# Performance work log

Hardware: AMD Instinct MI355X
Metric: run time of the kernel (lower is better)

Reference implementation:

```python
import jax, jax.numpy as jnp
import numpy as np

BASIS_N = 3            # Cl(3,0): 3 generators, euclidean metric e_i^2 = +1
BASIS_DIM = 1 << BASIS_N  # 8


def _geometric_product_table(n=BASIS_N):
    """G[i, j, k] such that e_i * e_j = sum_k G[i,j,k] e_k for blades indexed by bitmask."""
    dim = 1 << n
    G = np.zeros((dim, dim, dim), dtype=np.float32)
    for a in range(dim):
        for b in range(dim):
            # canonical reordering sign (count transpositions to sort basis vectors)
            s, t = 0, a >> 1
            while t:
                s += bin(t & b).count('1')
                t >>= 1
            sign = -1.0 if (s & 1) else 1.0
            G[a, b, a ^ b] = sign  # euclidean metric: squared generators contribute +1
    return G


def setup_inputs() -> dict:
    key = jax.random.key(0)
    kx, kw, kb = jax.random.split(key, 3)
    B, Cin, Cout, D, H, Wd, K = 8, 8, 8, 48, 48, 48, 3
    x = jax.random.normal(kx, (B, Cin, BASIS_DIM, D, H, Wd), dtype=jnp.float32)
    # W: [k0, k1, k2, in_channels, out_channels, basis_dim]
    W = jax.random.normal(kw, (K, K, K, Cin, Cout, BASIS_DIM), dtype=jnp.float32) * 0.05
    b = jax.random.normal(kb, (Cout, BASIS_DIM), dtype=jnp.float32) * 0.05
    G = jnp.asarray(_geometric_product_table())
    return {"x": x, "W": W, "b": b, "G": G}


def reference(x, W, b, G):
    # out[b,o,k,d,h,w] = sum_{i,j,c,m,l,v} G[i,j,k] * x[b,c,i,d+m,h+l,w+v] * W[m,l,v,c,o,j] + b[o,k]
    # Fold the GA multiplication table into the weights, then run a single dense 3D conv
    # over the fused (channel*basis) axis -- avoids the im2col unfold intermediate.
    k0, k1, k2, cin, cout, bd = W.shape
    B, C, I, D, H, Wd = x.shape
    Wt = jnp.einsum('ijk,mlvcoj->okcimlv', G, W)          # [o, k, c, i, m, l, v]
    xr = x.reshape(B, C * I, D, H, Wd)                    # fuse channel & basis-in
    kern = Wt.reshape(cout * bd, C * I, k0, k1, k2)       # fuse out-channel & basis-out
    out = jax.lax.conv_general_dilated(
        xr, kern, window_strides=(1, 1, 1), padding='VALID',
        dimension_numbers=('NCDHW', 'OIDHW', 'NCDHW'))
    out = out.reshape(B, cout, bd, *out.shape[2:])        # [B, o, k, d, h, w]
    return out + b[None, :, :, None, None, None]
```

## Files before the change

### kernel.cpp

```cpp
#include <hip/hip_runtime.h>


namespace {

constexpr int DIN = 48, DOUT = 46;
constexpr size_t X_ELEMS = 8ull * 8 * 8 * DIN * DIN * DIN;
constexpr size_t XBF_BYTES = X_ELEMS * 2;
constexpr int APK_ELEMS = 54 * 4 * 64 * 8;
constexpr int ROW_SHORTS = 2 * 4 * 48 * 8;
constexpr int ROW_BYTES = ROW_SHORTS * 2;

__host__ __device__ constexpr int popc_(int v) { int c = 0; while (v) { c += v & 1; v >>= 1; } return c; }
__host__ __device__ inline float ga_sign(int a, int b) {
  int s = 0;
  for (int t = a >> 1; t; t >>= 1) s += popc_(t & b);
  return (s & 1) ? -1.0f : 1.0f;
}

__device__ inline unsigned short f2bf(float f) {
  unsigned u = __builtin_bit_cast(unsigned, f);
  u += 0x7fffu + ((u >> 16) & 1u);
  return (unsigned short)(u >> 16);
}

__device__ inline void gload_lds16(const void* g, void* l) {
  __builtin_amdgcn_global_load_lds(
      (const __attribute__((address_space(1))) unsigned int*)g,
      (__attribute__((address_space(3))) unsigned int*)l, 16, 0, 0);
}

using frag  = __attribute__((ext_vector_type(8))) short;
using f32x4 = __attribute__((ext_vector_type(4))) float;

__global__ __launch_bounds__(256) void cvt_x(const float* __restrict__ x,
                                             unsigned short* __restrict__ xt) {
  const int bid = blockIdx.x;
  const int yg = bid % 6, bz = bid / 6;
  const int b = bz / 48, z = bz % 48;
  const int tid = threadIdx.x;
  __shared__ __attribute__((aligned(16))) unsigned short T[8 * ROW_SHORTS];
  const float* src = x + (size_t)b * 64 * 110592 + (size_t)z * 2304 + (size_t)yg * 384;
#pragma unroll
  for (int it = 0; it < 24; ++it) {
    const int i = it * 256 + tid;
    const int k = i / 96, j = i - k * 96;
    const int y = j / 12, x4 = j - y * 12;
    float4 f = *(const float4*)(src + (size_t)k * 110592 + y * 48 + x4 * 4);
    const int cb = k >> 5, q = (k >> 3) & 3, t = k & 7;
    const int basek = ((y * 2 + cb) * 4 + q) * 384 + t;
    unsigned short bfv[4] = {f2bf(f.x), f2bf(f.y), f2bf(f.z), f2bf(f.w)};
#pragma unroll
    for (int dx = 0; dx < 4; ++dx) {
      const int xx = x4 * 4 + dx;
      T[basek + ((xx ^ y) << 3)] = bfv[dx];
    }
  }
  __syncthreads();
  uint4* dst = (uint4*)(xt + ((size_t)bz * 48 + yg * 8) * ROW_SHORTS);
#pragma unroll
  for (int it = 0; it < 12; ++it) {
    const int C = it * 256 + tid;
    const int y = C / 384;
    const unsigned byteoff = (unsigned)(C * 16) ^ (unsigned)(y << 4);
    dst[C] = *(const uint4*)((const char*)T + byteoff);
  }
}

__global__ __launch_bounds__(256) void build_apk(const float* __restrict__ W,
                                                 unsigned short* __restrict__ Apk) {
  int e = blockIdx.x * 256 + threadIdx.x;
  int t  = e & 7;
  int mi = (e >> 3) & 63;
  int q  = (e >> 9) & 3;
  int s  = e >> 11;
  int cb = s & 1, mlv = s >> 1;
  int v = mlv % 3, l = (mlv / 3) % 3, m = mlv / 9;
  int kl = cb * 32 + q * 8 + t;
  int c = kl >> 3, i = kl & 7;
  int o = mi >> 3, kb = mi & 7, j = i ^ kb;
  float val = ga_sign(i, j) * W[((((m * 3 + l) * 3 + v) * 8 + c) * 8 + o) * 8 + j];
  Apk[e] = f2bf(val);
}

__global__ __launch_bounds__(256, 2) void gpconv_mfma(
    const unsigned short* __restrict__ xt,
    const unsigned short* __restrict__ Apk,
    const float* __restrict__ bias,
    float* __restrict__ out)
{
  const int d = blockIdx.x, hg = blockIdx.y, b = blockIdx.z;
  const int h0 = hg * 8;
  const int tid = threadIdx.x;
  const int wv = tid >> 6;
  const int lane = tid & 63, r = lane & 15, q = lane >> 4;

  __shared__ __attribute__((aligned(16))) unsigned short Xs[10 * ROW_SHORTS + 32];

  f32x4 acc[4][2][3];
#pragma unroll
  for (int ms = 0; ms < 4; ++ms)
#pragma unroll
    for (int row = 0; row < 2; ++row)
#pragma unroll
      for (int nt = 0; nt < 3; ++nt) acc[ms][row][nt] = (f32x4){0.f, 0.f, 0.f, 0.f};

  const unsigned short* Apl = Apk + q * 512 + r * 8;

  auto stage_half = [&](int zin, int cb) {
    const size_t R0 = (size_t)(b * 48 + zin) * 48 + h0;
#pragma unroll
    for (int i = 0; i < 3; ++i) {
      const int row = wv + i * 4;
      if (row < 10) {
        const char* g = (const char*)xt + (R0 + row) * ROW_BYTES + cb * 3072 + (size_t)lane * 16;
        unsigned loff = (unsigned)__builtin_amdgcn_readfirstlane(row * ROW_BYTES + cb * 3072);
#pragma unroll
        for (int ip = 0; ip < 3; ++ip)
          gload_lds16(g + ip * 1024, (char*)Xs + loff + ip * 1024);
      }
    }
  };

  auto compute_half = [&](int m, int cb) {
    const unsigned short* Xb = Xs + cb * 1536 + q * 384;
#pragma unroll
    for (int l = 0; l < 3; ++l) {
#pragma unroll
      for (int v = 0; v < 3; ++v) {
        const int mlv = (m * 3 + l) * 3 + v;
        frag a[4];
#pragma unroll
        for (int ms = 0; ms < 4; ++ms)
          a[ms] = *(const frag*)(Apl + (size_t)mlv * 4096 + cb * 2048 + ms * 128);
        frag bfr[2][3];
#pragma unroll
        for (int row = 0; row < 2; ++row) {
          const unsigned short* Xrow = Xb + (wv * 2 + row + l) * ROW_SHORTS + (r + v) * 8;
#pragma unroll
          for (int nt = 0; nt < 3; ++nt)
            bfr[row][nt] = *(const frag*)(Xrow + nt * 128);
        }
#pragma unroll
        for (int ms = 0; ms < 4; ++ms)
#pragma unroll
          for (int row = 0; row < 2; ++row)
#pragma unroll
            for (int nt = 0; nt < 3; ++nt)
              acc[ms][row][nt] = __builtin_amdgcn_mfma_f32_16x16x32_bf16(
                  a[ms], bfr[row][nt], acc[ms][row][nt], 0, 0, 0);
      }
    }
  };

  stage_half(d, 0);
  stage_half(d, 1);
  __syncthreads();
#pragma unroll 1
  for (int m = 0; m < 3; ++m) {
    compute_half(m, 0);
    __syncthreads();
    if (m < 2) stage_half(d + m + 1, 0);
    compute_half(m, 1);
    __syncthreads();
    if (m < 2) stage_half(d + m + 1, 1);
  }

#pragma unroll
  for (int row = 0; row < 2; ++row) {
    const int y = h0 + wv * 2 + row;
    if (y < DOUT) {
#pragma unroll
      for (int ms = 0; ms < 4; ++ms) {
#pragma unroll
        for (int nt = 0; nt < 3; ++nt) {
          const int w = nt * 16 + r;
          if (w < DOUT) {
#pragma unroll
            for (int reg = 0; reg < 4; ++reg) {
              const int mrow = ms * 16 + q * 4 + reg;
              const size_t oidx = (((size_t)(b * 64 + mrow) * DOUT + d) * DOUT + y) * DOUT + w;
              out[oidx] = acc[ms][row][nt][reg] + bias[mrow];
            }
          }
        }
      }
    }
  }
}

}

extern "C" void kernel_launch(void* const* d_in, const int* in_sizes, int n_in,
                              void* d_out, int out_size, void* d_ws, size_t ws_size,
                              hipStream_t stream) {
  const float* x    = (const float*)d_in[0];
  const float* W    = (const float*)d_in[1];
  const float* bias = (const float*)d_in[2];
  float* out = (float*)d_out;

  unsigned short* xt  = (unsigned short*)d_ws;
  unsigned short* Apk = (unsigned short*)((char*)d_ws + XBF_BYTES);

  cvt_x<<<8 * 48 * 6, 256, 0, stream>>>(x, xt);
  build_apk<<<APK_ELEMS / 256, 256, 0, stream>>>(W, Apk);

  dim3 grid(DOUT, 6, 8);
  gpconv_mfma<<<grid, 256, 0, stream>>>(xt, Apk, bias, out);
}
```

Baseline: 588.4 us.

## Overlap LDS staging with MFMA, double-buffer fragments, remap blocks across XCDs

The conv kernel now issues global-to-LDS staging of the next input slice partway through the current half's MFMA loop, so it no longer sits on a barrier. Fragment loads are double-buffered across the 9 (l,v) steps, and the MFMA bursts are wrapped in raised wave priority. The block index is permuted so consecutive blocks land on the same XCD. The conversion kernel is also restructured to write packed 4-element chunks to LDS and gather 8 channels per output vector. In exchange, register pressure rises from the doubled fragment buffers, and the staging order now depends on exact barrier placement.

```diff
diff --git a/kernel.cpp b/kernel.cpp
--- a/kernel.cpp
+++ b/kernel.cpp
@@ -36,9 +36,9 @@
                                              unsigned short* __restrict__ xt) {
   const int bid = blockIdx.x;
   const int yg = bid % 6, bz = bid / 6;
-  const int b = bz / 48, z = bz % 48;
+  const int b = bz / 48, z = bz - b * 48;
   const int tid = threadIdx.x;
-  __shared__ __attribute__((aligned(16))) unsigned short T[8 * ROW_SHORTS];
+  __shared__ __attribute__((aligned(16))) unsigned short T[64 * 8 * 48];
   const float* src = x + (size_t)b * 64 * 110592 + (size_t)z * 2304 + (size_t)yg * 384;
 #pragma unroll
   for (int it = 0; it < 24; ++it) {
@@ -46,23 +46,25 @@
     const int k = i / 96, j = i - k * 96;
     const int y = j / 12, x4 = j - y * 12;
     float4 f = *(const float4*)(src + (size_t)k * 110592 + y * 48 + x4 * 4);
-    const int cb = k >> 5, q = (k >> 3) & 3, t = k & 7;
-    const int basek = ((y * 2 + cb) * 4 + q) * 384 + t;
-    unsigned short bfv[4] = {f2bf(f.x), f2bf(f.y), f2bf(f.z), f2bf(f.w)};
-#pragma unroll
-    for (int dx = 0; dx < 4; ++dx) {
-      const int xx = x4 * 4 + dx;
-      T[basek + ((xx ^ y) << 3)] = bfv[dx];
-    }
+    uint2 p;
+    p.x = (unsigned)f2bf(f.x) | ((unsigned)f2bf(f.y) << 16);
+    p.y = (unsigned)f2bf(f.z) | ((unsigned)f2bf(f.w) << 16);
+    *(uint2*)&T[(k * 8 + y) * 48 + x4 * 4] = p;
   }
   __syncthreads();
   uint4* dst = (uint4*)(xt + ((size_t)bz * 48 + yg * 8) * ROW_SHORTS);
 #pragma unroll
   for (int it = 0; it < 12; ++it) {
     const int C = it * 256 + tid;
-    const int y = C / 384;
-    const unsigned byteoff = (unsigned)(C * 16) ^ (unsigned)(y << 4);
-    dst[C] = *(const uint4*)((const char*)T + byteoff);
+    const int y = C / 384, rem = C - y * 384;
+    const int kq = rem / 48, xx = rem - kq * 48;
+    const unsigned short* p0 = &T[(kq * 64 + y) * 48 + xx];
+    const unsigned s0 = p0[0],    s1 = p0[384],  s2 = p0[768],  s3 = p0[1152];
+    const unsigned s4 = p0[1536], s5 = p0[1920], s6 = p0[2304], s7 = p0[2688];
+    uint4 o;
+    o.x = s0 | (s1 << 16); o.y = s2 | (s3 << 16);
+    o.z = s4 | (s5 << 16); o.w = s6 | (s7 << 16);
+    dst[C] = o;
   }
 }
 
@@ -88,7 +90,11 @@
     const float* __restrict__ bias,
     float* __restrict__ out)
 {
-  const int d = blockIdx.x, hg = blockIdx.y, b = blockIdx.z;
+  const int fid0 = blockIdx.x + 46 * (blockIdx.y + 6 * blockIdx.z);
+  const int fid = (fid0 & 7) * 276 + (fid0 >> 3);
+  const int d = fid % 46;
+  const int t6 = fid / 46;
+  const int hg = t6 % 6, b = t6 / 6;
   const int h0 = hg * 8;
   const int tid = threadIdx.x;
   const int wv = tid >> 6;
@@ -121,34 +127,46 @@
     }
   };
 
-  auto compute_half = [&](int m, int cb) {
+  auto compute_half = [&](int m, int cb, bool do_stage, int stage_z, int stage_cb) {
     const unsigned short* Xb = Xs + cb * 1536 + q * 384;
-#pragma unroll
-    for (int l = 0; l < 3; ++l) {
-#pragma unroll
-      for (int v = 0; v < 3; ++v) {
-        const int mlv = (m * 3 + l) * 3 + v;
-        frag a[4];
+    const unsigned short* Ab = Apl + (size_t)m * 9 * 4096 + cb * 2048;
+    frag a[2][4];
+    frag bfr[2][2][3];
+#pragma unroll
+    for (int ms = 0; ms < 4; ++ms) a[0][ms] = *(const frag*)(Ab + ms * 128);
+#pragma unroll
+    for (int row = 0; row < 2; ++row) {
+      const unsigned short* Xrow = Xb + (wv * 2 + row) * ROW_SHORTS + r * 8;
+#pragma unroll
+      for (int nt = 0; nt < 3; ++nt) bfr[0][row][nt] = *(const frag*)(Xrow + nt * 128);
+    }
+#pragma unroll
+    for (int s = 0; s < 9; ++s) {
+      const int cur = s & 1, nxt = cur ^ 1;
+      if (s < 8) {
+        const int l = (s + 1) / 3, v = (s + 1) - l * 3;
 #pragma unroll
         for (int ms = 0; ms < 4; ++ms)
-          a[ms] = *(const frag*)(Apl + (size_t)mlv * 4096 + cb * 2048 + ms * 128);
-        frag bfr[2][3];
+          a[nxt][ms] = *(const frag*)(Ab + (s + 1) * 4096 + ms * 128);
 #pragma unroll
         for (int row = 0; row < 2; ++row) {
           const unsigned short* Xrow = Xb + (wv * 2 + row + l) * ROW_SHORTS + (r + v) * 8;
 #pragma unroll
           for (int nt = 0; nt < 3; ++nt)
-            bfr[row][nt] = *(const frag*)(Xrow + nt * 128);
+            bfr[nxt][row][nt] = *(const frag*)(Xrow + nt * 128);
         }
-#pragma unroll
-        for (int ms = 0; ms < 4; ++ms)
-#pragma unroll
-          for (int row = 0; row < 2; ++row)
-#pragma unroll
-            for (int nt = 0; nt < 3; ++nt)
-              acc[ms][row][nt] = __builtin_amdgcn_mfma_f32_16x16x32_bf16(
-                  a[ms], bfr[row][nt], acc[ms][row][nt], 0, 0, 0);
       }
+      if (s == 2 && do_stage) stage_half(stage_z, stage_cb);
+      __builtin_amdgcn_s_setprio(1);
+#pragma unroll
+      for (int ms = 0; ms < 4; ++ms)
+#pragma unroll
+        for (int row = 0; row < 2; ++row)
+#pragma unroll
+          for (int nt = 0; nt < 3; ++nt)
+            acc[ms][row][nt] = __builtin_amdgcn_mfma_f32_16x16x32_bf16(
+                a[cur][ms], bfr[cur][row][nt], acc[ms][row][nt], 0, 0, 0);
+      __builtin_amdgcn_s_setprio(0);
     }
   };
 
@@ -157,12 +175,10 @@
   __syncthreads();
 #pragma unroll 1
   for (int m = 0; m < 3; ++m) {
-    compute_half(m, 0);
+    compute_half(m, 0, m >= 1, d + m, 1);
     __syncthreads();
-    if (m < 2) stage_half(d + m + 1, 0);
-    compute_half(m, 1);
+    compute_half(m, 1, m < 2, d + m + 1, 0);
     __syncthreads();
-    if (m < 2) stage_half(d + m + 1, 1);
   }
 
 #pragma unroll
```

Result: faster. 532.2 us (-9.6%).
